# Optimization experiments

Hardware: AMD Instinct MI355X
Metric: run time of the kernel (lower is better)

The kernel has to match this reference:

```python
import jax, jax.numpy as jnp
import numpy as np

N_NODES = 20000
N_EDGES = 320000
IN_CH = 256
HID_CH = 256   # 2 * out_channels
OUT_CH = 128


def gcn_conv(x, edge_index, W, b, n_nodes):
    """PyG GCNConv: linear transform, add self-loops, sym-normalized scatter-add."""
    x = x @ W  # [N, C_out]
    loop = jnp.arange(n_nodes, dtype=edge_index.dtype)
    row = jnp.concatenate([edge_index[0], loop])  # source nodes
    col = jnp.concatenate([edge_index[1], loop])  # destination nodes
    deg = jax.ops.segment_sum(jnp.ones_like(col, dtype=x.dtype), col,
                              num_segments=n_nodes)
    deg_inv_sqrt = jnp.where(deg > 0, jax.lax.rsqrt(deg), 0.0)
    norm = deg_inv_sqrt[row] * deg_inv_sqrt[col]  # [E+N]
    msg = x[row] * norm[:, None]                  # gather + scale
    out = jax.ops.segment_sum(msg, col, num_segments=n_nodes)  # scatter-add
    return out + b


def setup_inputs() -> dict:
    key = jax.random.key(0)
    k1, k2, k3, k4, k5 = jax.random.split(key, 5)
    doc_embeds = jax.random.normal(k1, (N_NODES, IN_CH), dtype=jnp.float32)
    edge_index = jax.random.randint(k2, (2, N_EDGES), 0, N_NODES, dtype=jnp.int64)
    # Glorot-style init for GCN weights, zero bias (PyG defaults)
    s1 = 1.0 / np.sqrt(IN_CH)
    s2 = 1.0 / np.sqrt(HID_CH)
    W1 = jax.random.uniform(k3, (IN_CH, HID_CH), jnp.float32, -s1, s1)
    b1 = jnp.zeros((HID_CH,), jnp.float32)
    W2 = jax.random.uniform(k4, (HID_CH, OUT_CH), jnp.float32, -s2, s2)
    b2 = jnp.zeros((OUT_CH,), jnp.float32)
    return {"doc_embeds": doc_embeds, "edge_index": edge_index,
            "W1": W1, "b1": b1, "W2": W2, "b2": b2}


def reference(doc_embeds, edge_index, W1, b1, W2, b2):
    n = doc_embeds.shape[0]
    x = jax.nn.relu(gcn_conv(doc_embeds, edge_index, W1, b1, n))
    x = gcn_conv(x, edge_index, W2, b2, n)
    return x
```

## Files before the change

### kernel.cpp

```cpp
#include <hip/hip_runtime.h>
#include <math.h>

#define N_NODES 20000
#define N_EDGES 320000
#define IN_CH   256
#define HID_CH  256
#define OUT_CH  128
#define CAP     64
#define GK      256

typedef __attribute__((ext_vector_type(8))) unsigned short ushort8;
typedef __attribute__((ext_vector_type(4))) unsigned short ushort4v;
typedef __attribute__((ext_vector_type(4))) float floatx4;
typedef __attribute__((ext_vector_type(2))) float floatx2;
typedef __attribute__((ext_vector_type(2))) _Float16 half2v;
typedef __attribute__((ext_vector_type(8))) _Float16 half8;

__global__ __launch_bounds__(256)
void prep_kernel(const float* __restrict__ W1, const float* __restrict__ W2,
                 _Float16* __restrict__ W1t, _Float16* __restrict__ W2t,
                 const int* __restrict__ row, const int* __restrict__ col,
                 int* __restrict__ deg, unsigned short* __restrict__ srcs) {
    const int g = blockIdx.x * blockDim.x + threadIdx.x;
    const int gsz = gridDim.x * blockDim.x;
    for (int t = g; t < (IN_CH * HID_CH) / 16; t += gsz) {
        int n = t >> 4;
        int kc = (t & 15) * 16;
        half8 h0, h1;
#pragma unroll
        for (int j = 0; j < 8; ++j) {
            h0[j] = (_Float16)W1[(size_t)(kc + j) * HID_CH + n];
            h1[j] = (_Float16)W1[(size_t)(kc + 8 + j) * HID_CH + n];
        }
        *(half8*)(W1t + (size_t)n * IN_CH + kc)     = h0;
        *(half8*)(W1t + (size_t)n * IN_CH + kc + 8) = h1;
    }
    for (int t = g; t < (HID_CH * OUT_CH) / 16; t += gsz) {
        int n = t >> 4;
        int kc = (t & 15) * 16;
        half8 h0, h1;
#pragma unroll
        for (int j = 0; j < 8; ++j) {
            h0[j] = (_Float16)W2[(size_t)(kc + j) * OUT_CH + n];
            h1[j] = (_Float16)W2[(size_t)(kc + 8 + j) * OUT_CH + n];
        }
        *(half8*)(W2t + (size_t)n * HID_CH + kc)     = h0;
        *(half8*)(W2t + (size_t)n * HID_CH + kc + 8) = h1;
    }
    for (int i = g; i < N_EDGES; i += gsz) {
        int c = col[i];
        int r = row[i];
        int p = atomicAdd(&deg[c], 1);
        srcs[(size_t)c * CAP + p] = (unsigned short)r;
    }
}

__global__ __launch_bounds__(256, 2)
void gemm1_kernel(const float* __restrict__ Afp, const _Float16* __restrict__ Bt,
                  const int* __restrict__ deg, _Float16* __restrict__ C, int M, int N) {
    __shared__ _Float16 As[64][36];
    __shared__ _Float16 Bs[128][36];
    const int tid = threadIdx.x;
    const int m0 = blockIdx.y * 64;
    const int n0 = blockIdx.x * 128;
    const int lane = tid & 63;
    const int wave = tid >> 6;
    const int wr = (wave >> 1) * 32;
    const int wc = (wave & 1) * 64;
    const int lm = lane & 15;
    const int lk = (lane >> 4) * 8;

    floatx4 acc[2][4];
#pragma unroll
    for (int i = 0; i < 2; ++i)
#pragma unroll
        for (int j = 0; j < 4; ++j) acc[i][j] = (floatx4){0.f, 0.f, 0.f, 0.f};

    const int ar  = tid >> 2;
    const int ako = (tid & 3) * 8;

    for (int k0 = 0; k0 < GK; k0 += 32) {
        {
            half8 va = {};
            if (m0 + ar < M) {
                const float* ap = Afp + (size_t)(m0 + ar) * GK + k0 + ako;
                float4 f0 = *(const float4*)ap;
                float4 f1 = *(const float4*)(ap + 4);
                va[0] = (_Float16)f0.x; va[1] = (_Float16)f0.y;
                va[2] = (_Float16)f0.z; va[3] = (_Float16)f0.w;
                va[4] = (_Float16)f1.x; va[5] = (_Float16)f1.y;
                va[6] = (_Float16)f1.z; va[7] = (_Float16)f1.w;
            }
            *(half8*)&As[ar][ako] = va;
        }
#pragma unroll
        for (int c = 0; c < 2; ++c) {
            int ch = tid + c * 256;
            int r  = ch >> 2;
            int ko = (ch & 3) * 8;
            *(half8*)&Bs[r][ko] = *(const half8*)(Bt + (size_t)(n0 + r) * GK + k0 + ko);
        }
        __syncthreads();

        half8 ah[2];
#pragma unroll
        for (int i = 0; i < 2; ++i)
            ah[i] = *(const half8*)&As[wr + i * 16 + lm][lk];
#pragma unroll
        for (int j = 0; j < 4; ++j) {
            half8 bh = *(const half8*)&Bs[wc + j * 16 + lm][lk];
#pragma unroll
            for (int i = 0; i < 2; ++i)
                acc[i][j] = __builtin_amdgcn_mfma_f32_16x16x32_f16(ah[i], bh, acc[i][j], 0, 0, 0);
        }
        __syncthreads();
    }

#pragma unroll
    for (int i = 0; i < 2; ++i) {
#pragma unroll
        for (int r = 0; r < 4; ++r) {
            int rowi = m0 + wr + i * 16 + (lane >> 4) * 4 + r;
            if (rowi < M) {
                float dr = 1.0f / sqrtf((float)(deg[rowi] + 1));
#pragma unroll
                for (int j = 0; j < 4; ++j) {
                    C[(size_t)rowi * N + n0 + wc + j * 16 + lm] = (_Float16)(dr * acc[i][j][r]);
                }
            }
        }
    }
}

__global__ __launch_bounds__(256, 2)
void gemm2_fused_kernel(const _Float16* __restrict__ X, const int* __restrict__ deg,
                        const unsigned short* __restrict__ srcs,
                        const float* __restrict__ b1, const _Float16* __restrict__ Bt,
                        _Float16* __restrict__ C) {
    __shared__ _Float16 As[64][36];
    __shared__ _Float16 Bs[128][36];
    const int tid = threadIdx.x;
    const int m0 = blockIdx.x * 64;
    const int lane = tid & 63;
    const int wave = tid >> 6;
    const int wr = (wave >> 1) * 32;
    const int wc = (wave & 1) * 64;
    const int lm = lane & 15;
    const int lk = (lane >> 4) * 8;

    const int ar  = tid >> 2;
    const int ako = (tid & 3) * 8;
    const int node = m0 + ar;
    const bool valid = node < N_NODES;
    const int cnt = valid ? deg[node] : 0;
    const float dc = 1.0f / sqrtf((float)(cnt + 1));
    const size_t beg = (size_t)node * CAP;

    floatx4 acc[2][4];
#pragma unroll
    for (int i = 0; i < 2; ++i)
#pragma unroll
        for (int j = 0; j < 4; ++j) acc[i][j] = (floatx4){0.f, 0.f, 0.f, 0.f};

    for (int k0 = 0; k0 < GK; k0 += 32) {
        {
            const _Float16* Xb = X + k0 + ako;
            float a[8] = {0.f, 0.f, 0.f, 0.f, 0.f, 0.f, 0.f, 0.f};
            int e = 0;
            for (; e + 4 <= cnt; e += 4) {
                ushort4v s4 = *(const ushort4v*)(srcs + beg + e);
                half8 v0 = *(const half8*)(Xb + (size_t)s4.x * GK);
                half8 v1 = *(const half8*)(Xb + (size_t)s4.y * GK);
                half8 v2 = *(const half8*)(Xb + (size_t)s4.z * GK);
                half8 v3 = *(const half8*)(Xb + (size_t)s4.w * GK);
#pragma unroll
                for (int j = 0; j < 8; ++j)
                    a[j] += (float)v0[j] + (float)v1[j] + (float)v2[j] + (float)v3[j];
            }
            for (; e < cnt; ++e) {
                int r = srcs[beg + e];
                half8 v = *(const half8*)(Xb + (size_t)r * GK);
#pragma unroll
                for (int j = 0; j < 8; ++j) a[j] += (float)v[j];
            }
            half8 hv = {};
            if (valid) {
                half8 self = *(const half8*)(Xb + (size_t)node * GK);
                float4 bb0 = *(const float4*)(b1 + k0 + ako);
                float4 bb1 = *(const float4*)(b1 + k0 + ako + 4);
                float bj[8] = {bb0.x, bb0.y, bb0.z, bb0.w, bb1.x, bb1.y, bb1.z, bb1.w};
#pragma unroll
                for (int j = 0; j < 8; ++j)
                    hv[j] = (_Float16)fmaxf(dc * (a[j] + (float)self[j]) + bj[j], 0.f);
            }
            *(half8*)&As[ar][ako] = hv;
        }
#pragma unroll
        for (int c = 0; c < 2; ++c) {
            int ch = tid + c * 256;
            int r  = ch >> 2;
            int ko = (ch & 3) * 8;
            *(half8*)&Bs[r][ko] = *(const half8*)(Bt + (size_t)r * GK + k0 + ko);
        }
        __syncthreads();

        half8 ah[2];
#pragma unroll
        for (int i = 0; i < 2; ++i)
            ah[i] = *(const half8*)&As[wr + i * 16 + lm][lk];
#pragma unroll
        for (int j = 0; j < 4; ++j) {
            half8 bh = *(const half8*)&Bs[wc + j * 16 + lm][lk];
#pragma unroll
            for (int i = 0; i < 2; ++i)
                acc[i][j] = __builtin_amdgcn_mfma_f32_16x16x32_f16(ah[i], bh, acc[i][j], 0, 0, 0);
        }
        __syncthreads();
    }

#pragma unroll
    for (int i = 0; i < 2; ++i) {
#pragma unroll
        for (int r = 0; r < 4; ++r) {
            int rowi = m0 + wr + i * 16 + (lane >> 4) * 4 + r;
            if (rowi < N_NODES) {
                float dr = 1.0f / sqrtf((float)(deg[rowi] + 1));
#pragma unroll
                for (int j = 0; j < 4; ++j) {
                    C[(size_t)rowi * OUT_CH + wc + j * 16 + lm] = (_Float16)(dr * acc[i][j][r]);
                }
            }
        }
    }
}

template <int C, int NSLICE>
__global__ __launch_bounds__(256)
void gather_out_kernel(const _Float16* __restrict__ X, const int* __restrict__ deg,
                       const unsigned short* __restrict__ srcs,
                       const float* __restrict__ bias, float* __restrict__ outf, int n) {
    constexpr int SW = C / NSLICE;
    static_assert(SW == 32, "slice must be 32 channels");
    const int slice = blockIdx.x % NSLICE;
    const int ngrp  = blockIdx.x / NSLICE;
    const int wave = threadIdx.x >> 6;
    const int lane = threadIdx.x & 63;
    const int g  = lane >> 4;
    const int sl = lane & 15;
    const int node = ngrp * 16 + wave * 4 + g;
    if (node >= n) return;
    const int choff = slice * SW + sl * 2;
    const size_t beg = (size_t)node * CAP;
    const int cnt = deg[node];

    float a0 = 0.f, a1 = 0.f;
    int e = 0;
    for (; e + 8 <= cnt; e += 8) {
        ushort8 s8 = *(const ushort8*)(srcs + beg + e);
        half2v v0 = *(const half2v*)(X + (size_t)s8[0] * C + choff);
        half2v v1 = *(const half2v*)(X + (size_t)s8[1] * C + choff);
        half2v v2 = *(const half2v*)(X + (size_t)s8[2] * C + choff);
        half2v v3 = *(const half2v*)(X + (size_t)s8[3] * C + choff);
        half2v v4 = *(const half2v*)(X + (size_t)s8[4] * C + choff);
        half2v v5 = *(const half2v*)(X + (size_t)s8[5] * C + choff);
        half2v v6 = *(const half2v*)(X + (size_t)s8[6] * C + choff);
        half2v v7 = *(const half2v*)(X + (size_t)s8[7] * C + choff);
        a0 += (float)v0.x + (float)v1.x + (float)v2.x + (float)v3.x
            + (float)v4.x + (float)v5.x + (float)v6.x + (float)v7.x;
        a1 += (float)v0.y + (float)v1.y + (float)v2.y + (float)v3.y
            + (float)v4.y + (float)v5.y + (float)v6.y + (float)v7.y;
    }
    for (; e + 4 <= cnt; e += 4) {
        ushort4v s4 = *(const ushort4v*)(srcs + beg + e);
        half2v v0 = *(const half2v*)(X + (size_t)s4.x * C + choff);
        half2v v1 = *(const half2v*)(X + (size_t)s4.y * C + choff);
        half2v v2 = *(const half2v*)(X + (size_t)s4.z * C + choff);
        half2v v3 = *(const half2v*)(X + (size_t)s4.w * C + choff);
        a0 += (float)v0.x + (float)v1.x + (float)v2.x + (float)v3.x;
        a1 += (float)v0.y + (float)v1.y + (float)v2.y + (float)v3.y;
    }
    for (; e < cnt; ++e) {
        int r = srcs[beg + e];
        half2v v = *(const half2v*)(X + (size_t)r * C + choff);
        a0 += (float)v.x; a1 += (float)v.y;
    }

    const float dc = 1.0f / sqrtf((float)(cnt + 1));
    half2v vsh = *(const half2v*)(X + (size_t)node * C + choff);
    float2 bb = *(const float2*)(bias + choff);

    float o0 = dc * (a0 + (float)vsh.x) + bb.x;
    float o1 = dc * (a1 + (float)vsh.y) + bb.y;

    floatx2 o = {o0, o1};
    __builtin_nontemporal_store(o, (floatx2*)(outf + (size_t)node * C + choff));
}

extern "C" void kernel_launch(void* const* d_in, const int* in_sizes, int n_in,
                              void* d_out, int out_size, void* d_ws, size_t ws_size,
                              hipStream_t stream) {
    const float* doc_embeds = (const float*)d_in[0];
    const int*   edge_index = (const int*)d_in[1];
    const float* W1 = (const float*)d_in[2];
    const float* b1 = (const float*)d_in[3];
    const float* W2 = (const float*)d_in[4];
    const float* b2 = (const float*)d_in[5];
    float* out = (float*)d_out;

    const int* row = edge_index;
    const int* col = edge_index + N_EDGES;

    char* ws = (char*)d_ws;
    auto align_up = [](size_t x) { return (x + 255) / 256 * 256; };

    _Float16* X1s = (_Float16*)(ws);
    _Float16* X2s = (_Float16*)(ws + align_up((size_t)N_NODES * HID_CH * 2));
    char* meta = (char*)(ws + 2 * align_up((size_t)N_NODES * HID_CH * 2));
    _Float16* W1t = (_Float16*)(meta); meta += align_up((size_t)IN_CH * HID_CH * 2);
    _Float16* W2t = (_Float16*)(meta); meta += align_up((size_t)HID_CH * OUT_CH * 2);
    int*            deg  = (int*)(meta);            meta += align_up((size_t)N_NODES * 4);
    unsigned short* srcs = (unsigned short*)(meta);

    hipMemsetAsync(deg, 0, (size_t)N_NODES * 4, stream);
    prep_kernel<<<(N_EDGES + 255) / 256, 256, 0, stream>>>(
        W1, W2, W1t, W2t, row, col, deg, srcs);

    {
        dim3 grid(HID_CH / 128, (N_NODES + 63) / 64);
        gemm1_kernel<<<grid, 256, 0, stream>>>(
            doc_embeds, W1t, deg, X1s, N_NODES, HID_CH);
    }

    gemm2_fused_kernel<<<(N_NODES + 63) / 64, 256, 0, stream>>>(
        X1s, deg, srcs, b1, W2t, X2s);

    gather_out_kernel<OUT_CH, 4><<<((N_NODES + 15) / 16) * 4, 256, 0, stream>>>(
        X2s, deg, srcs, b2, out, N_NODES);
}
```

Measured before the change: 183.9 us.

## Overlap edge bucketing with GEMM1 and split fused aggregation into separate gather kernel

```diff
diff --git a/kernel.cpp b/kernel.cpp
--- a/kernel.cpp
+++ b/kernel.cpp
@@ -8,6 +8,7 @@
 #define OUT_CH  128
 #define CAP     64
 #define GK      256
+#define NEB     256
 
 typedef __attribute__((ext_vector_type(8))) unsigned short ushort8;
 typedef __attribute__((ext_vector_type(4))) unsigned short ushort4v;
@@ -17,12 +18,12 @@
 typedef __attribute__((ext_vector_type(8))) _Float16 half8;
 
 __global__ __launch_bounds__(256)
-void prep_kernel(const float* __restrict__ W1, const float* __restrict__ W2,
-                 _Float16* __restrict__ W1t, _Float16* __restrict__ W2t,
-                 const int* __restrict__ row, const int* __restrict__ col,
-                 int* __restrict__ deg, unsigned short* __restrict__ srcs) {
+void prep0_kernel(const float* __restrict__ W1, const float* __restrict__ W2,
+                  _Float16* __restrict__ W1t, _Float16* __restrict__ W2t,
+                  int* __restrict__ deg) {
     const int g = blockIdx.x * blockDim.x + threadIdx.x;
     const int gsz = gridDim.x * blockDim.x;
+    for (int i = g; i < N_NODES; i += gsz) deg[i] = 0;
     for (int t = g; t < (IN_CH * HID_CH) / 16; t += gsz) {
         int n = t >> 4;
         int kc = (t & 15) * 16;
@@ -47,22 +48,29 @@
         *(half8*)(W2t + (size_t)n * HID_CH + kc)     = h0;
         *(half8*)(W2t + (size_t)n * HID_CH + kc + 8) = h1;
     }
-    for (int i = g; i < N_EDGES; i += gsz) {
-        int c = col[i];
-        int r = row[i];
-        int p = atomicAdd(&deg[c], 1);
-        srcs[(size_t)c * CAP + p] = (unsigned short)r;
-    }
 }
 
 __global__ __launch_bounds__(256, 2)
-void gemm1_kernel(const float* __restrict__ Afp, const _Float16* __restrict__ Bt,
-                  const int* __restrict__ deg, _Float16* __restrict__ C, int M, int N) {
+void gemm1_edge_kernel(const float* __restrict__ doc, const _Float16* __restrict__ Bt,
+                       const int* __restrict__ row, const int* __restrict__ col,
+                       int* __restrict__ deg, unsigned short* __restrict__ srcs,
+                       _Float16* __restrict__ X1s) {
     __shared__ _Float16 As[64][36];
     __shared__ _Float16 Bs[128][36];
+    const int bid = blockIdx.x;
     const int tid = threadIdx.x;
-    const int m0 = blockIdx.y * 64;
-    const int n0 = blockIdx.x * 128;
+    if (bid < NEB) {
+        for (int i = bid * 256 + tid; i < N_EDGES; i += NEB * 256) {
+            int c = col[i];
+            int r = row[i];
+            int p = atomicAdd(&deg[c], 1);
+            srcs[(size_t)c * CAP + p] = (unsigned short)r;
+        }
+        return;
+    }
+    const int t = bid - NEB;
+    const int m0 = (t >> 1) * 64;
+    const int n0 = (t & 1) * 128;
     const int lane = tid & 63;
     const int wave = tid >> 6;
     const int wr = (wave >> 1) * 32;
@@ -82,8 +90,8 @@
     for (int k0 = 0; k0 < GK; k0 += 32) {
         {
             half8 va = {};
-            if (m0 + ar < M) {
-                const float* ap = Afp + (size_t)(m0 + ar) * GK + k0 + ako;
+            if (m0 + ar < N_NODES) {
+                const float* ap = doc + (size_t)(m0 + ar) * GK + k0 + ako;
                 float4 f0 = *(const float4*)ap;
                 float4 f1 = *(const float4*)(ap + 4);
                 va[0] = (_Float16)f0.x; va[1] = (_Float16)f0.y;
@@ -121,22 +129,74 @@
 #pragma unroll
         for (int r = 0; r < 4; ++r) {
             int rowi = m0 + wr + i * 16 + (lane >> 4) * 4 + r;
-            if (rowi < M) {
-                float dr = 1.0f / sqrtf((float)(deg[rowi] + 1));
+            if (rowi < N_NODES) {
 #pragma unroll
                 for (int j = 0; j < 4; ++j) {
-                    C[(size_t)rowi * N + n0 + wc + j * 16 + lm] = (_Float16)(dr * acc[i][j][r]);
+                    X1s[(size_t)rowi * HID_CH + n0 + wc + j * 16 + lm] = (_Float16)acc[i][j][r];
                 }
             }
         }
     }
 }
 
+template <int C, int NSLICE>
+__global__ __launch_bounds__(256)
+void gather_h1_kernel(const _Float16* __restrict__ X, const int* __restrict__ deg,
+                      const unsigned short* __restrict__ srcs,
+                      const float* __restrict__ bias, _Float16* __restrict__ outh, int n) {
+    constexpr int SW = C / NSLICE;
+    static_assert(SW == 32, "slice must be 32 channels");
+    const int slice = blockIdx.x % NSLICE;
+    const int ngrp  = blockIdx.x / NSLICE;
+    const int wave = threadIdx.x >> 6;
+    const int lane = threadIdx.x & 63;
+    const int g  = lane >> 4;
+    const int sl = lane & 15;
+    const int node = ngrp * 16 + wave * 4 + g;
+    if (node >= n) return;
+    const int choff = slice * SW + sl * 2;
+    const size_t beg = (size_t)node * CAP;
+    const int cnt = deg[node];
+
+    float a0 = 0.f, a1 = 0.f;
+    int e = 0;
+    for (; e + 4 <= cnt; e += 4) {
+        ushort4v s4 = *(const ushort4v*)(srcs + beg + e);
+        float w0 = __builtin_amdgcn_rsqf((float)(deg[s4.x] + 1));
+        float w1 = __builtin_amdgcn_rsqf((float)(deg[s4.y] + 1));
+        float w2 = __builtin_amdgcn_rsqf((float)(deg[s4.z] + 1));
+        float w3 = __builtin_amdgcn_rsqf((float)(deg[s4.w] + 1));
+        half2v v0 = *(const half2v*)(X + (size_t)s4.x * C + choff);
+        half2v v1 = *(const half2v*)(X + (size_t)s4.y * C + choff);
+        half2v v2 = *(const half2v*)(X + (size_t)s4.z * C + choff);
+        half2v v3 = *(const half2v*)(X + (size_t)s4.w * C + choff);
+        a0 = fmaf(w0, (float)v0.x, fmaf(w1, (float)v1.x, fmaf(w2, (float)v2.x, fmaf(w3, (float)v3.x, a0))));
+        a1 = fmaf(w0, (float)v0.y, fmaf(w1, (float)v1.y, fmaf(w2, (float)v2.y, fmaf(w3, (float)v3.y, a1))));
+    }
+    for (; e < cnt; ++e) {
+        int r = srcs[beg + e];
+        float w = __builtin_amdgcn_rsqf((float)(deg[r] + 1));
+        half2v v = *(const half2v*)(X + (size_t)r * C + choff);
+        a0 = fmaf(w, (float)v.x, a0);
+        a1 = fmaf(w, (float)v.y, a1);
+    }
+
+    const float dc = __builtin_amdgcn_rsqf((float)(cnt + 1));
+    half2v vsh = *(const half2v*)(X + (size_t)node * C + choff);
+    float2 bb = *(const float2*)(bias + choff);
+
+    float o0 = dc * (a0 + dc * (float)vsh.x) + bb.x;
+    float o1 = dc * (a1 + dc * (float)vsh.y) + bb.y;
+
+    half2v h;
+    h.x = (_Float16)fmaxf(o0, 0.f);
+    h.y = (_Float16)fmaxf(o1, 0.f);
+    *(half2v*)(outh + (size_t)node * C + choff) = h;
+}
+
 __global__ __launch_bounds__(256, 2)
-void gemm2_fused_kernel(const _Float16* __restrict__ X, const int* __restrict__ deg,
-                        const unsigned short* __restrict__ srcs,
-                        const float* __restrict__ b1, const _Float16* __restrict__ Bt,
-                        _Float16* __restrict__ C) {
+void gemm2_kernel(const _Float16* __restrict__ Ah, const _Float16* __restrict__ Bt,
+                  const int* __restrict__ deg, _Float16* __restrict__ C) {
     __shared__ _Float16 As[64][36];
     __shared__ _Float16 Bs[128][36];
     const int tid = threadIdx.x;
@@ -148,52 +208,21 @@
     const int lm = lane & 15;
     const int lk = (lane >> 4) * 8;
 
+    floatx4 acc[2][4];
+#pragma unroll
+    for (int i = 0; i < 2; ++i)
+#pragma unroll
+        for (int j = 0; j < 4; ++j) acc[i][j] = (floatx4){0.f, 0.f, 0.f, 0.f};
+
     const int ar  = tid >> 2;
     const int ako = (tid & 3) * 8;
-    const int node = m0 + ar;
-    const bool valid = node < N_NODES;
-    const int cnt = valid ? deg[node] : 0;
-    const float dc = 1.0f / sqrtf((float)(cnt + 1));
-    const size_t beg = (size_t)node * CAP;
-
-    floatx4 acc[2][4];
-#pragma unroll
-    for (int i = 0; i < 2; ++i)
-#pragma unroll
-        for (int j = 0; j < 4; ++j) acc[i][j] = (floatx4){0.f, 0.f, 0.f, 0.f};
 
     for (int k0 = 0; k0 < GK; k0 += 32) {
         {
-            const _Float16* Xb = X + k0 + ako;
-            float a[8] = {0.f, 0.f, 0.f, 0.f, 0.f, 0.f, 0.f, 0.f};
-            int e = 0;
-            for (; e + 4 <= cnt; e += 4) {
-                ushort4v s4 = *(const ushort4v*)(srcs + beg + e);
-                half8 v0 = *(const half8*)(Xb + (size_t)s4.x * GK);
-                half8 v1 = *(const half8*)(Xb + (size_t)s4.y * GK);
-                half8 v2 = *(const half8*)(Xb + (size_t)s4.z * GK);
-                half8 v3 = *(const half8*)(Xb + (size_t)s4.w * GK);
-#pragma unroll
-                for (int j = 0; j < 8; ++j)
-                    a[j] += (float)v0[j] + (float)v1[j] + (float)v2[j] + (float)v3[j];
-            }
-            for (; e < cnt; ++e) {
-                int r = srcs[beg + e];
-                half8 v = *(const half8*)(Xb + (size_t)r * GK);
-#pragma unroll
-                for (int j = 0; j < 8; ++j) a[j] += (float)v[j];
-            }
-            half8 hv = {};
-            if (valid) {
-                half8 self = *(const half8*)(Xb + (size_t)node * GK);
-                float4 bb0 = *(const float4*)(b1 + k0 + ako);
-                float4 bb1 = *(const float4*)(b1 + k0 + ako + 4);
-                float bj[8] = {bb0.x, bb0.y, bb0.z, bb0.w, bb1.x, bb1.y, bb1.z, bb1.w};
-#pragma unroll
-                for (int j = 0; j < 8; ++j)
-                    hv[j] = (_Float16)fmaxf(dc * (a[j] + (float)self[j]) + bj[j], 0.f);
-            }
-            *(half8*)&As[ar][ako] = hv;
+            half8 va = {};
+            if (m0 + ar < N_NODES)
+                va = *(const half8*)(Ah + (size_t)(m0 + ar) * GK + k0 + ako);
+            *(half8*)&As[ar][ako] = va;
         }
 #pragma unroll
         for (int c = 0; c < 2; ++c) {
@@ -314,25 +343,23 @@
     auto align_up = [](size_t x) { return (x + 255) / 256 * 256; };
 
     _Float16* X1s = (_Float16*)(ws);
-    _Float16* X2s = (_Float16*)(ws + align_up((size_t)N_NODES * HID_CH * 2));
+    _Float16* H1  = (_Float16*)(ws + align_up((size_t)N_NODES * HID_CH * 2));
+    _Float16* X2s = X1s;
     char* meta = (char*)(ws + 2 * align_up((size_t)N_NODES * HID_CH * 2));
     _Float16* W1t = (_Float16*)(meta); meta += align_up((size_t)IN_CH * HID_CH * 2);
     _Float16* W2t = (_Float16*)(meta); meta += align_up((size_t)HID_CH * OUT_CH * 2);
     int*            deg  = (int*)(meta);            meta += align_up((size_t)N_NODES * 4);
     unsigned short* srcs = (unsigned short*)(meta);
 
-    hipMemsetAsync(deg, 0, (size_t)N_NODES * 4, stream);
-    prep_kernel<<<(N_EDGES + 255) / 256, 256, 0, stream>>>(
-        W1, W2, W1t, W2t, row, col, deg, srcs);
-
-    {
-        dim3 grid(HID_CH / 128, (N_NODES + 63) / 64);
-        gemm1_kernel<<<grid, 256, 0, stream>>>(
-            doc_embeds, W1t, deg, X1s, N_NODES, HID_CH);
-    }
-
-    gemm2_fused_kernel<<<(N_NODES + 63) / 64, 256, 0, stream>>>(
-        X1s, deg, srcs, b1, W2t, X2s);
+    prep0_kernel<<<256, 256, 0, stream>>>(W1, W2, W1t, W2t, deg);
+
+    gemm1_edge_kernel<<<NEB + 626, 256, 0, stream>>>(
+        doc_embeds, W1t, row, col, deg, srcs, X1s);
+
+    gather_h1_kernel<HID_CH, 8><<<((N_NODES + 15) / 16) * 8, 256, 0, stream>>>(
+        X1s, deg, srcs, b1, H1, N_NODES);
+
+    gemm2_kernel<<<(N_NODES + 63) / 64, 256, 0, stream>>>(H1, W2t, deg, X2s);
 
     gather_out_kernel<OUT_CH, 4><<<((N_NODES + 15) / 16) * 4, 256, 0, stream>>>(
         X2s, deg, srcs, b2, out, N_NODES);
```

New measurement: 164.8 us. 1.12x faster.
